# Kernel optimization log

Measured on AMD Instinct MI355X. Metric: run time of the kernel, lower is better.

## Reference

```python
import jax, jax.numpy as jnp
import numpy as np

N_NODES = 100000
N_EDGES = 1600000
N_GRAPHS = 64
F = 128  # feature_dim == hidden_dim == embedding_dim
NUM_CONVS = 3


def _layernorm(h, g, b, eps=1e-5):
    mu = jnp.mean(h, axis=-1, keepdims=True)
    var = jnp.var(h, axis=-1, keepdims=True)
    return (h - mu) * jax.lax.rsqrt(var + eps) * g + b


def setup_inputs() -> dict:
    key = jax.random.key(0)
    ks = jax.random.split(key, 12)
    s = 1.0 / np.sqrt(F)
    return {
        "x": jax.random.normal(ks[0], (N_NODES, F), jnp.float32),
        "edge_index": jax.random.randint(ks[1], (2, N_EDGES), 0, N_NODES, jnp.int32),
        "batch_vec": jnp.sort(jax.random.randint(ks[2], (N_NODES,), 0, N_GRAPHS, jnp.int32)),
        "gammas": 1.0 + 0.1 * jax.random.normal(ks[3], (N_GRAPHS, NUM_CONVS), jnp.float32),
        "betas": 0.1 * jax.random.normal(ks[4], (N_GRAPHS, NUM_CONVS), jnp.float32),
        "pre_W0": s * jax.random.normal(ks[5], (F, F), jnp.float32),
        "pre_b0": jnp.zeros((F,), jnp.float32),
        "pre_W1": s * jax.random.normal(ks[6], (F, F), jnp.float32),
        "pre_b1": jnp.zeros((F,), jnp.float32),
        "gin_W": s * jax.random.normal(ks[7], (NUM_CONVS, 2, F, F), jnp.float32),
        "gin_b": jnp.zeros((NUM_CONVS, 2, F), jnp.float32),
        "post_W0": (1.0 / np.sqrt(5 * F)) * jax.random.normal(ks[8], (5 * F, F), jnp.float32),
        "post_b0": jnp.zeros((F,), jnp.float32),
        "post_ln_g": jnp.ones((F,), jnp.float32),
        "post_ln_b": jnp.zeros((F,), jnp.float32),
        "post_W1": s * jax.random.normal(ks[9], (F, F), jnp.float32),
        "post_b1": jnp.zeros((F,), jnp.float32),
    }


def reference(x, edge_index, batch_vec, gammas, betas,
              pre_W0, pre_b0, pre_W1, pre_b1,
              gin_W, gin_b,
              post_W0, post_b0, post_ln_g, post_ln_b, post_W1, post_b1):
    n = x.shape[0]
    src, dst = edge_index[0], edge_index[1]

    # preprocess MLP (2 layers, ReLU between, batch_norm='none')
    h = jnp.dot(jax.nn.relu(jnp.dot(x, pre_W0) + pre_b0), pre_W1) + pre_b1
    jump_xs = [x, h]

    # per-node FiLM coefficients (repeat_interleave over sorted batch == gather)
    g_nodes = gammas[batch_vec]  # [N, num_convs]
    b_nodes = betas[batch_vec]   # [N, num_convs]

    for i in range(NUM_CONVS):
        # GINConv, eps=0: MLP(h_i + sum_{j->i} h_j)
        aggr = jax.ops.segment_sum(h[src], dst, num_segments=n)
        z = h + aggr
        h = jnp.dot(jax.nn.relu(jnp.dot(z, gin_W[i, 0]) + gin_b[i, 0]), gin_W[i, 1]) + gin_b[i, 1]
        # FiLM modulation
        h = h * g_nodes[:, i:i + 1] + b_nodes[:, i:i + 1]
        jump_xs.append(h)

    # jumping knowledge 'cat'
    h = jnp.concatenate(jump_xs, axis=-1)  # [N, feature + 4*hidden]

    # postprocess MLP with LayerNorm (batch_norm='layer'); dropout p=0 (eval)
    z = jnp.dot(h, post_W0) + post_b0
    z = jax.nn.relu(_layernorm(z, post_ln_g, post_ln_b))
    return jnp.dot(z, post_W1) + post_b1
```

## Files before the change

kernel.cpp:

```cpp
#include <hip/hip_runtime.h>

#define FDIM 128
constexpr int EP_NONE = 0, EP_RELU = 1, EP_FILM = 2, EP_LNRELU = 3;

struct Srcs { const float* p[5]; };


__global__ __launch_bounds__(256)
void k_hist(const int* __restrict__ dst, int* __restrict__ cnt, int E) {
  int e = blockIdx.x * 256 + threadIdx.x;
  if (e < E) atomicAdd(&cnt[dst[e]], 1);
}

__global__ __launch_bounds__(1024)
void k_scan_block(const int* __restrict__ cnt, int* __restrict__ scanned,
                  int* __restrict__ partials, int n) {
  __shared__ int sd[1024];
  int tid = threadIdx.x;
  int i = blockIdx.x * 1024 + tid;
  int v = (i < n) ? cnt[i] : 0;
  sd[tid] = v; __syncthreads();
  for (int off = 1; off < 1024; off <<= 1) {
    int t = (tid >= off) ? sd[tid - off] : 0;
    __syncthreads();
    sd[tid] += t;
    __syncthreads();
  }
  if (i < n) scanned[i] = sd[tid] - v;
  if (tid == 1023) partials[blockIdx.x] = sd[1023];
}

__global__ __launch_bounds__(128)
void k_scan_small(const int* __restrict__ partials, int* __restrict__ p2, int nb) {
  __shared__ int sd[128];
  int tid = threadIdx.x;
  int v = (tid < nb) ? partials[tid] : 0;
  sd[tid] = v; __syncthreads();
  for (int off = 1; off < 128; off <<= 1) {
    int t = (tid >= off) ? sd[tid - off] : 0;
    __syncthreads();
    sd[tid] += t;
    __syncthreads();
  }
  p2[tid] = sd[tid] - v;
}

__global__ __launch_bounds__(256)
void k_finalize(const int* __restrict__ scanned, const int* __restrict__ p2,
                int* __restrict__ indptr, int* __restrict__ cursor, int n, int E) {
  int i = blockIdx.x * 256 + threadIdx.x;
  if (i < n) {
    int v = scanned[i] + p2[i >> 10];
    indptr[i] = v;
    cursor[i] = v;
  }
  if (i == 0) indptr[n] = E;
}

__global__ __launch_bounds__(256)
void k_scatter(const int* __restrict__ src, const int* __restrict__ dst,
               int* __restrict__ cursor, int* __restrict__ eids, int E) {
  int e = blockIdx.x * 256 + threadIdx.x;
  if (e < E) {
    int p = atomicAdd(&cursor[dst[e]], 1);
    eids[p] = src[e];
  }
}


__global__ __launch_bounds__(256)
void k_aggr(const float* __restrict__ h, const int* __restrict__ indptr,
            const int* __restrict__ eids, float* __restrict__ z, int n) {
  int lane = threadIdx.x & 63;
  int node = blockIdx.x * 4 + (threadIdx.x >> 6);
  if (node >= n) return;
  float2 acc = *(const float2*)&h[(size_t)node * FDIM + lane * 2];
  int s = indptr[node], e = indptr[node + 1];
  for (int base = s; base < e; base += 64) {
    int cnt = min(64, e - base);
    int eid = (base + lane < e) ? eids[base + lane] : 0;
    for (int j = 0; j < cnt; ++j) {
      int sn = __shfl(eid, j, 64);
      float2 hv = *(const float2*)&h[(size_t)sn * FDIM + lane * 2];
      acc.x += hv.x; acc.y += hv.y;
    }
  }
  *(float2*)&z[(size_t)node * FDIM + lane * 2] = acc;
}


template<int NSRC, int EPI>
__global__ __launch_bounds__(256)
void k_gemm(Srcs srcs, const float* __restrict__ W, const float* __restrict__ bias,
            float* __restrict__ out, int n,
            const int* __restrict__ bvec, const float* __restrict__ gam,
            const float* __restrict__ bet, int conv,
            const float* __restrict__ lng, const float* __restrict__ lnb) {
  __shared__ float As[64][68];
  __shared__ float Ws[64 * FDIM];
  const int tid = threadIdx.x;
  const int tx = tid & 31;
  const int ty = tid >> 5;
  const int row0 = blockIdx.x * 64;
  const int sr = tid >> 2;
  const int sk = (tid & 3) * 16;

  float acc[8][4];
  #pragma unroll
  for (int i = 0; i < 8; ++i)
    #pragma unroll
    for (int j = 0; j < 4; ++j) acc[i][j] = 0.f;

  for (int js = 0; js < NSRC; ++js) {
    const float* __restrict__ A = srcs.p[js];
    #pragma unroll
    for (int cc = 0; cc < 2; ++cc) {
      const int kb = cc * 64;
      {
        const int gr = row0 + sr;
        const float* Ar = A + (size_t)gr * FDIM + kb + sk;
        #pragma unroll
        for (int t = 0; t < 4; ++t) {
          float4 v = {0.f, 0.f, 0.f, 0.f};
          if (gr < n) v = *(const float4*)(Ar + t * 4);
          const int k = sk + t * 4;
          As[k + 0][sr] = v.x; As[k + 1][sr] = v.y;
          As[k + 2][sr] = v.z; As[k + 3][sr] = v.w;
        }
      }
      {
        const float* Wg = W + (size_t)(js * FDIM + kb) * FDIM;
        #pragma unroll
        for (int t = 0; t < 8; ++t) {
          const int idx = tid * 4 + t * 1024;
          *(float4*)&Ws[idx] = *(const float4*)&Wg[idx];
        }
      }
      __syncthreads();
      #pragma unroll 8
      for (int kk = 0; kk < 64; ++kk) {
        const float4 w = *(const float4*)&Ws[kk * FDIM + tx * 4];
        const float4 a0 = *(const float4*)&As[kk][ty * 8];
        const float4 a1 = *(const float4*)&As[kk][ty * 8 + 4];
        const float a[8] = {a0.x, a0.y, a0.z, a0.w, a1.x, a1.y, a1.z, a1.w};
        #pragma unroll
        for (int i = 0; i < 8; ++i) {
          acc[i][0] = fmaf(a[i], w.x, acc[i][0]);
          acc[i][1] = fmaf(a[i], w.y, acc[i][1]);
          acc[i][2] = fmaf(a[i], w.z, acc[i][2]);
          acc[i][3] = fmaf(a[i], w.w, acc[i][3]);
        }
      }
      __syncthreads();
    }
  }

  const float4 bv = *(const float4*)&bias[tx * 4];

  if constexpr (EPI == EP_LNRELU) {
    float v[8][4], s[8], sq[8];
    #pragma unroll
    for (int i = 0; i < 8; ++i) {
      v[i][0] = acc[i][0] + bv.x; v[i][1] = acc[i][1] + bv.y;
      v[i][2] = acc[i][2] + bv.z; v[i][3] = acc[i][3] + bv.w;
      s[i] = 0.f; sq[i] = 0.f;
      #pragma unroll
      for (int j = 0; j < 4; ++j) { s[i] += v[i][j]; sq[i] += v[i][j] * v[i][j]; }
    }
    #pragma unroll
    for (int m = 1; m < 32; m <<= 1) {
      #pragma unroll
      for (int i = 0; i < 8; ++i) {
        s[i]  += __shfl_xor(s[i],  m, 64);
        sq[i] += __shfl_xor(sq[i], m, 64);
      }
    }
    const float4 g4 = *(const float4*)&lng[tx * 4];
    const float4 b4 = *(const float4*)&lnb[tx * 4];
    #pragma unroll
    for (int i = 0; i < 8; ++i) {
      const int r = row0 + ty * 8 + i;
      const float mu = s[i] * (1.f / FDIM);
      const float var = sq[i] * (1.f / FDIM) - mu * mu;
      const float rs = rsqrtf(var + 1e-5f);
      float4 o;
      o.x = fmaxf((v[i][0] - mu) * rs * g4.x + b4.x, 0.f);
      o.y = fmaxf((v[i][1] - mu) * rs * g4.y + b4.y, 0.f);
      o.z = fmaxf((v[i][2] - mu) * rs * g4.z + b4.z, 0.f);
      o.w = fmaxf((v[i][3] - mu) * rs * g4.w + b4.w, 0.f);
      if (r < n) *(float4*)&out[(size_t)r * FDIM + tx * 4] = o;
    }
  } else {
    #pragma unroll
    for (int i = 0; i < 8; ++i) {
      const int r = row0 + ty * 8 + i;
      if (r >= n) continue;
      float4 o;
      o.x = acc[i][0] + bv.x; o.y = acc[i][1] + bv.y;
      o.z = acc[i][2] + bv.z; o.w = acc[i][3] + bv.w;
      if constexpr (EPI == EP_RELU) {
        o.x = fmaxf(o.x, 0.f); o.y = fmaxf(o.y, 0.f);
        o.z = fmaxf(o.z, 0.f); o.w = fmaxf(o.w, 0.f);
      } else if constexpr (EPI == EP_FILM) {
        const int b = bvec[r];
        const float g = gam[b * 3 + conv];
        const float be = bet[b * 3 + conv];
        o.x = o.x * g + be; o.y = o.y * g + be;
        o.z = o.z * g + be; o.w = o.w * g + be;
      }
      *(float4*)&out[(size_t)r * FDIM + tx * 4] = o;
    }
  }
}


extern "C" void kernel_launch(void* const* d_in, const int* in_sizes, int n_in,
                              void* d_out, int out_size, void* d_ws, size_t ws_size,
                              hipStream_t stream) {
  const float* x       = (const float*)d_in[0];
  const int*   eidx    = (const int*)d_in[1];
  const int*   bvec    = (const int*)d_in[2];
  const float* gam     = (const float*)d_in[3];
  const float* bet     = (const float*)d_in[4];
  const float* pre_W0  = (const float*)d_in[5];
  const float* pre_b0  = (const float*)d_in[6];
  const float* pre_W1  = (const float*)d_in[7];
  const float* pre_b1  = (const float*)d_in[8];
  const float* gin_W   = (const float*)d_in[9];
  const float* gin_b   = (const float*)d_in[10];
  const float* post_W0 = (const float*)d_in[11];
  const float* post_b0 = (const float*)d_in[12];
  const float* lng     = (const float*)d_in[13];
  const float* lnb     = (const float*)d_in[14];
  const float* post_W1 = (const float*)d_in[15];
  const float* post_b1 = (const float*)d_in[16];

  const int n = in_sizes[0] / FDIM;
  const int E = in_sizes[1] / 2;
  const int* esrc = eidx;
  const int* edst = eidx + E;
  float* out = (float*)d_out;

  const size_t NF = (size_t)n * FDIM;
  float* fws = (float*)d_ws;
  float* h0  = fws;
  float* h1  = fws + NF;
  float* h2  = fws + 2 * NF;
  float* h3  = fws + 3 * NF;
  float* zb  = out;
  float* tmp = out;
  int* iws      = (int*)(fws + 4 * NF);
  int* counts   = iws;
  int* scanned  = iws + n;
  int* indptr   = iws + 2 * n;
  int* cursor   = iws + 3 * n + 1;
  int* partials = iws + 4 * n + 1;
  int* p2       = partials + 128;
  int* eids     = p2 + 128;

  hipMemsetAsync(counts, 0, (size_t)n * sizeof(int), stream);
  k_hist<<<(E + 255) / 256, 256, 0, stream>>>(edst, counts, E);
  const int nb = (n + 1023) / 1024;
  k_scan_block<<<nb, 1024, 0, stream>>>(counts, scanned, partials, n);
  k_scan_small<<<1, 128, 0, stream>>>(partials, p2, nb);
  k_finalize<<<(n + 255) / 256, 256, 0, stream>>>(scanned, p2, indptr, cursor, n, E);
  k_scatter<<<(E + 255) / 256, 256, 0, stream>>>(esrc, edst, cursor, eids, E);

  const int gb = (n + 63) / 64;

  Srcs sx{{x, nullptr, nullptr, nullptr, nullptr}};
  k_gemm<1, EP_RELU><<<gb, 256, 0, stream>>>(sx, pre_W0, pre_b0, tmp, n,
                                             nullptr, nullptr, nullptr, 0, nullptr, nullptr);
  Srcs st0{{tmp, nullptr, nullptr, nullptr, nullptr}};
  k_gemm<1, EP_NONE><<<gb, 256, 0, stream>>>(st0, pre_W1, pre_b1, h0, n,
                                             nullptr, nullptr, nullptr, 0, nullptr, nullptr);

  float* hprev = h0;
  float* houts[3] = {h1, h2, h3};
  for (int i = 0; i < 3; ++i) {
    k_aggr<<<(n + 3) / 4, 256, 0, stream>>>(hprev, indptr, eids, zb, n);
    Srcs sz{{zb, nullptr, nullptr, nullptr, nullptr}};
    k_gemm<1, EP_RELU><<<gb, 256, 0, stream>>>(
        sz, gin_W + (size_t)(i * 2) * FDIM * FDIM, gin_b + (size_t)(i * 2) * FDIM,
        tmp, n, nullptr, nullptr, nullptr, 0, nullptr, nullptr);
    Srcs st{{tmp, nullptr, nullptr, nullptr, nullptr}};
    k_gemm<1, EP_FILM><<<gb, 256, 0, stream>>>(
        st, gin_W + (size_t)(i * 2 + 1) * FDIM * FDIM, gin_b + (size_t)(i * 2 + 1) * FDIM,
        houts[i], n, bvec, gam, bet, i, nullptr, nullptr);
    hprev = houts[i];
  }

  Srcs sj{{x, h0, h1, h2, h3}};
  k_gemm<5, EP_LNRELU><<<gb, 256, 0, stream>>>(sj, post_W0, post_b0, tmp, n,
                                               nullptr, nullptr, nullptr, 0, lng, lnb);
  Srcs sf{{tmp, nullptr, nullptr, nullptr, nullptr}};
  k_gemm<1, EP_NONE><<<gb, 256, 0, stream>>>(sf, post_W1, post_b1, out, n,
                                             nullptr, nullptr, nullptr, 0, nullptr, nullptr);
}
```

Before: 1.396 ms.

## Replace FP32 SIMT GEMMs with split-bf16 MFMA kernels and unroll aggregation

Replaces the shared-memory FP32 FMA GEMM with an MFMA-based kernel using 16x16x32 bf16 instructions. Activations and weights are each split into hi and lo bf16 parts, and three products are accumulated to keep near-FP32 accuracy. A pre-pass kernel converts and transposes all 14 weight matrices into hi/lo bf16 buffers in workspace. The aggregation loop is also unrolled by four neighbours to raise memory-level parallelism. The costs are the extra conversion arithmetic and weight fragments read straight from global memory without LDS reuse, and the output stores are now scalar rather than vectorised.

```diff
diff --git a/kernel.cpp b/kernel.cpp
--- a/kernel.cpp
+++ b/kernel.cpp
@@ -1,9 +1,23 @@
 #include <hip/hip_runtime.h>
+#include <stdint.h>
 
 #define FDIM 128
 constexpr int EP_NONE = 0, EP_RELU = 1, EP_FILM = 2, EP_LNRELU = 3;
 
+typedef __attribute__((ext_vector_type(8))) short short8v;
+typedef __attribute__((ext_vector_type(4))) float f32x4;
+
 struct Srcs { const float* p[5]; };
+struct WPtrs { const float* p[14]; };
+
+__device__ inline short f2bf(float f) {
+  unsigned u = __float_as_uint(f);
+  u = (u + 0x7fffu + ((u >> 16) & 1u)) >> 16;
+  return (short)u;
+}
+__device__ inline float bf2f(short s) {
+  return __uint_as_float(((unsigned)(unsigned short)s) << 16);
+}
 
 
 __global__ __launch_bounds__(256)
@@ -79,7 +93,20 @@
   for (int base = s; base < e; base += 64) {
     int cnt = min(64, e - base);
     int eid = (base + lane < e) ? eids[base + lane] : 0;
-    for (int j = 0; j < cnt; ++j) {
+    int j = 0;
+    for (; j + 4 <= cnt; j += 4) {
+      int s0 = __shfl(eid, j, 64);
+      int s1 = __shfl(eid, j + 1, 64);
+      int s2 = __shfl(eid, j + 2, 64);
+      int s3 = __shfl(eid, j + 3, 64);
+      float2 v0 = *(const float2*)&h[(size_t)s0 * FDIM + lane * 2];
+      float2 v1 = *(const float2*)&h[(size_t)s1 * FDIM + lane * 2];
+      float2 v2 = *(const float2*)&h[(size_t)s2 * FDIM + lane * 2];
+      float2 v3 = *(const float2*)&h[(size_t)s3 * FDIM + lane * 2];
+      acc.x += v0.x + v1.x + v2.x + v3.x;
+      acc.y += v0.y + v1.y + v2.y + v3.y;
+    }
+    for (; j < cnt; ++j) {
       int sn = __shfl(eid, j, 64);
       float2 hv = *(const float2*)&h[(size_t)sn * FDIM + lane * 2];
       acc.x += hv.x; acc.y += hv.y;
@@ -89,127 +116,151 @@
 }
 
 
+__global__ __launch_bounds__(256)
+void k_wt(WPtrs wp, short* __restrict__ wtHi, short* __restrict__ wtLo) {
+  const int m = blockIdx.x;
+  const float* __restrict__ W = wp.p[m];
+  const int t = threadIdx.x;
+  #pragma unroll
+  for (int u = 0; u < 8; ++u) {
+    int chunk = t + u * 256;
+    int c = chunk >> 4, kc = chunk & 15;
+    short8v hi, lo;
+    #pragma unroll
+    for (int j = 0; j < 8; ++j) {
+      float w = W[(kc * 8 + j) * FDIM + c];
+      short h = f2bf(w);
+      hi[j] = h;
+      lo[j] = f2bf(w - bf2f(h));
+    }
+    int off = m * 16384 + c * FDIM + kc * 8;
+    *(short8v*)(wtHi + off) = hi;
+    *(short8v*)(wtLo + off) = lo;
+  }
+}
+
+
 template<int NSRC, int EPI>
 __global__ __launch_bounds__(256)
-void k_gemm(Srcs srcs, const float* __restrict__ W, const float* __restrict__ bias,
-            float* __restrict__ out, int n,
+void k_mfma(Srcs srcs, const short* __restrict__ wtHi, const short* __restrict__ wtLo,
+            int m0, const float* __restrict__ bias, float* __restrict__ out, int n,
             const int* __restrict__ bvec, const float* __restrict__ gam,
             const float* __restrict__ bet, int conv,
             const float* __restrict__ lng, const float* __restrict__ lnb) {
-  __shared__ float As[64][68];
-  __shared__ float Ws[64 * FDIM];
   const int tid = threadIdx.x;
-  const int tx = tid & 31;
-  const int ty = tid >> 5;
-  const int row0 = blockIdx.x * 64;
-  const int sr = tid >> 2;
-  const int sk = (tid & 3) * 16;
-
-  float acc[8][4];
+  const int lane = tid & 63;
+  const int w = tid >> 6;
+  const int lr = lane & 15;
+  const int lg = lane >> 4;
+  const int row0 = blockIdx.x * 128 + w * 32;
+
+  f32x4 acc[2][8];
   #pragma unroll
-  for (int i = 0; i < 8; ++i)
-    #pragma unroll
-    for (int j = 0; j < 4; ++j) acc[i][j] = 0.f;
+  for (int s = 0; s < 2; ++s)
+    #pragma unroll
+    for (int f = 0; f < 8; ++f) acc[s][f] = (f32x4){0.f, 0.f, 0.f, 0.f};
 
   for (int js = 0; js < NSRC; ++js) {
     const float* __restrict__ A = srcs.p[js];
-    #pragma unroll
-    for (int cc = 0; cc < 2; ++cc) {
-      const int kb = cc * 64;
-      {
-        const int gr = row0 + sr;
-        const float* Ar = A + (size_t)gr * FDIM + kb + sk;
+    const int wbase = (m0 + js) * 16384;
+    #pragma unroll
+    for (int k0i = 0; k0i < 4; ++k0i) {
+      const int k0 = k0i * 32;
+      short8v ah[2], al[2];
+      #pragma unroll
+      for (int s = 0; s < 2; ++s) {
+        const int r = row0 + s * 16 + lr;
+        float4 v0 = {0.f, 0.f, 0.f, 0.f}, v1 = {0.f, 0.f, 0.f, 0.f};
+        if (r < n) {
+          const float* Ar = A + (size_t)r * FDIM + k0 + lg * 8;
+          v0 = *(const float4*)Ar;
+          v1 = *(const float4*)(Ar + 4);
+        }
+        const float vv[8] = {v0.x, v0.y, v0.z, v0.w, v1.x, v1.y, v1.z, v1.w};
         #pragma unroll
-        for (int t = 0; t < 4; ++t) {
-          float4 v = {0.f, 0.f, 0.f, 0.f};
-          if (gr < n) v = *(const float4*)(Ar + t * 4);
-          const int k = sk + t * 4;
-          As[k + 0][sr] = v.x; As[k + 1][sr] = v.y;
-          As[k + 2][sr] = v.z; As[k + 3][sr] = v.w;
+        for (int j = 0; j < 8; ++j) {
+          short h = f2bf(vv[j]);
+          ah[s][j] = h;
+          al[s][j] = f2bf(vv[j] - bf2f(h));
         }
       }
-      {
-        const float* Wg = W + (size_t)(js * FDIM + kb) * FDIM;
+      #pragma unroll
+      for (int f = 0; f < 8; ++f) {
+        const int boff = wbase + (f * 16 + lr) * FDIM + k0 + lg * 8;
+        short8v bh = *(const short8v*)(wtHi + boff);
+        short8v bl = *(const short8v*)(wtLo + boff);
+        acc[0][f] = __builtin_amdgcn_mfma_f32_16x16x32_bf16(ah[0], bh, acc[0][f], 0, 0, 0);
+        acc[1][f] = __builtin_amdgcn_mfma_f32_16x16x32_bf16(ah[1], bh, acc[1][f], 0, 0, 0);
+        acc[0][f] = __builtin_amdgcn_mfma_f32_16x16x32_bf16(al[0], bh, acc[0][f], 0, 0, 0);
+        acc[1][f] = __builtin_amdgcn_mfma_f32_16x16x32_bf16(al[1], bh, acc[1][f], 0, 0, 0);
+        acc[0][f] = __builtin_amdgcn_mfma_f32_16x16x32_bf16(ah[0], bl, acc[0][f], 0, 0, 0);
+        acc[1][f] = __builtin_amdgcn_mfma_f32_16x16x32_bf16(ah[1], bl, acc[1][f], 0, 0, 0);
+      }
+    }
+  }
+
+  float bb[8];
+  #pragma unroll
+  for (int f = 0; f < 8; ++f) bb[f] = bias[f * 16 + lr];
+
+  if constexpr (EPI == EP_LNRELU) {
+    float gg[8], bn[8];
+    #pragma unroll
+    for (int f = 0; f < 8; ++f) { gg[f] = lng[f * 16 + lr]; bn[f] = lnb[f * 16 + lr]; }
+    #pragma unroll
+    for (int s = 0; s < 2; ++s) {
+      float sm[4] = {0.f, 0.f, 0.f, 0.f}, sq[4] = {0.f, 0.f, 0.f, 0.f};
+      #pragma unroll
+      for (int f = 0; f < 8; ++f)
         #pragma unroll
-        for (int t = 0; t < 8; ++t) {
-          const int idx = tid * 4 + t * 1024;
-          *(float4*)&Ws[idx] = *(const float4*)&Wg[idx];
+        for (int i = 0; i < 4; ++i) {
+          float v = acc[s][f][i] + bb[f];
+          acc[s][f][i] = v;
+          sm[i] += v; sq[i] += v * v;
+        }
+      #pragma unroll
+      for (int m = 1; m < 16; m <<= 1)
+        #pragma unroll
+        for (int i = 0; i < 4; ++i) {
+          sm[i] += __shfl_xor(sm[i], m, 64);
+          sq[i] += __shfl_xor(sq[i], m, 64);
+        }
+      #pragma unroll
+      for (int i = 0; i < 4; ++i) {
+        const int r = row0 + s * 16 + 4 * lg + i;
+        const float mu = sm[i] * (1.f / FDIM);
+        const float var = sq[i] * (1.f / FDIM) - mu * mu;
+        const float rs = rsqrtf(var + 1e-5f);
+        if (r < n) {
+          #pragma unroll
+          for (int f = 0; f < 8; ++f) {
+            float o = fmaxf((acc[s][f][i] - mu) * rs * gg[f] + bn[f], 0.f);
+            out[(size_t)r * FDIM + f * 16 + lr] = o;
+          }
         }
       }
-      __syncthreads();
-      #pragma unroll 8
-      for (int kk = 0; kk < 64; ++kk) {
-        const float4 w = *(const float4*)&Ws[kk * FDIM + tx * 4];
-        const float4 a0 = *(const float4*)&As[kk][ty * 8];
-        const float4 a1 = *(const float4*)&As[kk][ty * 8 + 4];
-        const float a[8] = {a0.x, a0.y, a0.z, a0.w, a1.x, a1.y, a1.z, a1.w};
+    }
+  } else {
+    #pragma unroll
+    for (int s = 0; s < 2; ++s)
+      #pragma unroll
+      for (int i = 0; i < 4; ++i) {
+        const int r = row0 + s * 16 + 4 * lg + i;
+        if (r >= n) continue;
+        float g = 1.f, be = 0.f;
+        if constexpr (EPI == EP_FILM) {
+          int b = bvec[r];
+          g = gam[b * 3 + conv];
+          be = bet[b * 3 + conv];
+        }
         #pragma unroll
-        for (int i = 0; i < 8; ++i) {
-          acc[i][0] = fmaf(a[i], w.x, acc[i][0]);
-          acc[i][1] = fmaf(a[i], w.y, acc[i][1]);
-          acc[i][2] = fmaf(a[i], w.z, acc[i][2]);
-          acc[i][3] = fmaf(a[i], w.w, acc[i][3]);
+        for (int f = 0; f < 8; ++f) {
+          float o = acc[s][f][i] + bb[f];
+          if constexpr (EPI == EP_RELU) o = fmaxf(o, 0.f);
+          if constexpr (EPI == EP_FILM) o = o * g + be;
+          out[(size_t)r * FDIM + f * 16 + lr] = o;
         }
       }
-      __syncthreads();
-    }
-  }
-
-  const float4 bv = *(const float4*)&bias[tx * 4];
-
-  if constexpr (EPI == EP_LNRELU) {
-    float v[8][4], s[8], sq[8];
-    #pragma unroll
-    for (int i = 0; i < 8; ++i) {
-      v[i][0] = acc[i][0] + bv.x; v[i][1] = acc[i][1] + bv.y;
-      v[i][2] = acc[i][2] + bv.z; v[i][3] = acc[i][3] + bv.w;
-      s[i] = 0.f; sq[i] = 0.f;
-      #pragma unroll
-      for (int j = 0; j < 4; ++j) { s[i] += v[i][j]; sq[i] += v[i][j] * v[i][j]; }
-    }
-    #pragma unroll
-    for (int m = 1; m < 32; m <<= 1) {
-      #pragma unroll
-      for (int i = 0; i < 8; ++i) {
-        s[i]  += __shfl_xor(s[i],  m, 64);
-        sq[i] += __shfl_xor(sq[i], m, 64);
-      }
-    }
-    const float4 g4 = *(const float4*)&lng[tx * 4];
-    const float4 b4 = *(const float4*)&lnb[tx * 4];
-    #pragma unroll
-    for (int i = 0; i < 8; ++i) {
-      const int r = row0 + ty * 8 + i;
-      const float mu = s[i] * (1.f / FDIM);
-      const float var = sq[i] * (1.f / FDIM) - mu * mu;
-      const float rs = rsqrtf(var + 1e-5f);
-      float4 o;
-      o.x = fmaxf((v[i][0] - mu) * rs * g4.x + b4.x, 0.f);
-      o.y = fmaxf((v[i][1] - mu) * rs * g4.y + b4.y, 0.f);
-      o.z = fmaxf((v[i][2] - mu) * rs * g4.z + b4.z, 0.f);
-      o.w = fmaxf((v[i][3] - mu) * rs * g4.w + b4.w, 0.f);
-      if (r < n) *(float4*)&out[(size_t)r * FDIM + tx * 4] = o;
-    }
-  } else {
-    #pragma unroll
-    for (int i = 0; i < 8; ++i) {
-      const int r = row0 + ty * 8 + i;
-      if (r >= n) continue;
-      float4 o;
-      o.x = acc[i][0] + bv.x; o.y = acc[i][1] + bv.y;
-      o.z = acc[i][2] + bv.z; o.w = acc[i][3] + bv.w;
-      if constexpr (EPI == EP_RELU) {
-        o.x = fmaxf(o.x, 0.f); o.y = fmaxf(o.y, 0.f);
-        o.z = fmaxf(o.z, 0.f); o.w = fmaxf(o.w, 0.f);
-      } else if constexpr (EPI == EP_FILM) {
-        const int b = bvec[r];
-        const float g = gam[b * 3 + conv];
-        const float be = bet[b * 3 + conv];
-        o.x = o.x * g + be; o.y = o.y * g + be;
-        o.z = o.z * g + be; o.w = o.w * g + be;
-      }
-      *(float4*)&out[(size_t)r * FDIM + tx * 4] = o;
-    }
   }
 }
 
@@ -257,6 +308,17 @@
   int* partials = iws + 4 * n + 1;
   int* p2       = partials + 128;
   int* eids     = p2 + 128;
+  uintptr_t wtb = ((uintptr_t)(eids + E) + 15) & ~(uintptr_t)15;
+  short* wtHi = (short*)wtb;
+  short* wtLo = wtHi + 14 * 16384;
+
+  WPtrs wp;
+  wp.p[0] = pre_W0;
+  wp.p[1] = pre_W1;
+  for (int i = 0; i < 6; ++i) wp.p[2 + i] = gin_W + (size_t)i * 16384;
+  for (int j = 0; j < 5; ++j) wp.p[8 + j] = post_W0 + (size_t)j * 16384;
+  wp.p[13] = post_W1;
+  k_wt<<<14, 256, 0, stream>>>(wp, wtHi, wtLo);
 
   hipMemsetAsync(counts, 0, (size_t)n * sizeof(int), stream);
   k_hist<<<(E + 255) / 256, 256, 0, stream>>>(edst, counts, E);
@@ -266,13 +328,13 @@
   k_finalize<<<(n + 255) / 256, 256, 0, stream>>>(scanned, p2, indptr, cursor, n, E);
   k_scatter<<<(E + 255) / 256, 256, 0, stream>>>(esrc, edst, cursor, eids, E);
 
-  const int gb = (n + 63) / 64;
+  const int gb = (n + 127) / 128;
 
   Srcs sx{{x, nullptr, nullptr, nullptr, nullptr}};
-  k_gemm<1, EP_RELU><<<gb, 256, 0, stream>>>(sx, pre_W0, pre_b0, tmp, n,
+  k_mfma<1, EP_RELU><<<gb, 256, 0, stream>>>(sx, wtHi, wtLo, 0, pre_b0, tmp, n,
                                              nullptr, nullptr, nullptr, 0, nullptr, nullptr);
   Srcs st0{{tmp, nullptr, nullptr, nullptr, nullptr}};
-  k_gemm<1, EP_NONE><<<gb, 256, 0, stream>>>(st0, pre_W1, pre_b1, h0, n,
+  k_mfma<1, EP_NONE><<<gb, 256, 0, stream>>>(st0, wtHi, wtLo, 1, pre_b1, h0, n,
                                              nullptr, nullptr, nullptr, 0, nullptr, nullptr);
 
   float* hprev = h0;
@@ -280,20 +342,20 @@
   for (int i = 0; i < 3; ++i) {
     k_aggr<<<(n + 3) / 4, 256, 0, stream>>>(hprev, indptr, eids, zb, n);
     Srcs sz{{zb, nullptr, nullptr, nullptr, nullptr}};
-    k_gemm<1, EP_RELU><<<gb, 256, 0, stream>>>(
-        sz, gin_W + (size_t)(i * 2) * FDIM * FDIM, gin_b + (size_t)(i * 2) * FDIM,
-        tmp, n, nullptr, nullptr, nullptr, 0, nullptr, nullptr);
+    k_mfma<1, EP_RELU><<<gb, 256, 0, stream>>>(
+        sz, wtHi, wtLo, 2 + 2 * i, gin_b + (size_t)(2 * i) * FDIM, tmp, n,
+        nullptr, nullptr, nullptr, 0, nullptr, nullptr);
     Srcs st{{tmp, nullptr, nullptr, nullptr, nullptr}};
-    k_gemm<1, EP_FILM><<<gb, 256, 0, stream>>>(
-        st, gin_W + (size_t)(i * 2 + 1) * FDIM * FDIM, gin_b + (size_t)(i * 2 + 1) * FDIM,
-        houts[i], n, bvec, gam, bet, i, nullptr, nullptr);
+    k_mfma<1, EP_FILM><<<gb, 256, 0, stream>>>(
+        st, wtHi, wtLo, 3 + 2 * i, gin_b + (size_t)(2 * i + 1) * FDIM, houts[i], n,
+        bvec, gam, bet, i, nullptr, nullptr);
     hprev = houts[i];
   }
 
   Srcs sj{{x, h0, h1, h2, h3}};
-  k_gemm<5, EP_LNRELU><<<gb, 256, 0, stream>>>(sj, post_W0, post_b0, tmp, n,
+  k_mfma<5, EP_LNRELU><<<gb, 256, 0, stream>>>(sj, wtHi, wtLo, 8, post_b0, tmp, n,
                                                nullptr, nullptr, nullptr, 0, lng, lnb);
   Srcs sf{{tmp, nullptr, nullptr, nullptr, nullptr}};
-  k_gemm<1, EP_NONE><<<gb, 256, 0, stream>>>(sf, post_W1, post_b1, out, n,
+  k_mfma<1, EP_NONE><<<gb, 256, 0, stream>>>(sf, wtHi, wtLo, 13, post_b1, out, n,
                                              nullptr, nullptr, nullptr, 0, nullptr, nullptr);
 }
```

After: 1.403 ms. No clear change (+0.5%).
